# Optimization experiments

Measured on AMD Instinct MI355X. Metric: run time of the kernel, lower is better.

## Reference

```python
import jax, jax.numpy as jnp
import numpy as np

B, S, H = 4, 2048, 1024
NH, HD = 16, 64
ROPE_THETA = 160000.0
SCALE = HD ** -0.5


def _rope_cos_sin(position_ids, dim, theta):
    # neox-style rotary: frequencies over half the head dim
    inv_freq = 1.0 / (theta ** (jnp.arange(0, dim, 2, dtype=jnp.float32) / dim))  # [dim/2]
    freqs = position_ids.astype(jnp.float32)[..., None] * inv_freq  # [B,S,dim/2]
    return jnp.cos(freqs), jnp.sin(freqs)


def _apply_rope(x, cos, sin):
    # x: [B,S,NH,HD]; neox style: rotate halves
    d2 = x.shape[-1] // 2
    x1, x2 = x[..., :d2], x[..., d2:]
    c = cos[:, :, None, :]
    s = sin[:, :, None, :]
    return jnp.concatenate([x1 * c - x2 * s, x2 * c + x1 * s], axis=-1)


def setup_inputs() -> dict:
    key = jax.random.key(0)
    k1, k2, k3 = jax.random.split(key, 3)
    hidden_states = jax.random.normal(k1, (B, S, H), dtype=jnp.float32)
    position_ids = jnp.tile(jnp.arange(S, dtype=jnp.int32)[None, :], (B, 1))
    Wqkv = jax.random.normal(k2, (3 * H, H), dtype=jnp.float32) * (H ** -0.5)
    Wo = jax.random.normal(k3, (H, H), dtype=jnp.float32) * (H ** -0.5)
    return {"hidden_states": hidden_states, "position_ids": position_ids,
            "Wqkv": Wqkv, "Wo": Wo}


def reference(hidden_states, position_ids, Wqkv, Wo):
    # fused QKV projection
    qkv = jnp.einsum('bsh,oh->bso', hidden_states, Wqkv)  # [B,S,3H]
    q, k, v = jnp.split(qkv, 3, axis=-1)
    q = q.reshape(B, S, NH, HD)
    k = k.reshape(B, S, NH, HD)
    v = v.reshape(B, S, NH, HD)
    # rotary embedding (neox style)
    cos, sin = _rope_cos_sin(position_ids, HD, ROPE_THETA)
    q = _apply_rope(q, cos, sin)
    k = _apply_rope(k, cos, sin)
    # full bidirectional (encoder-only, global layer) attention
    scores = jnp.einsum('bqhd,bkhd->bhqk', q, k) * SCALE  # [B,NH,S,S]
    probs = jax.nn.softmax(scores, axis=-1)
    ctx = jnp.einsum('bhqk,bkhd->bqhd', probs, v).reshape(B, S, H)
    # output projection
    return jnp.einsum('bsh,oh->bso', ctx, Wo)
```

## Files before the change

### kernel.cpp

```cpp
#include <hip/hip_runtime.h>
#include <hip/hip_bf16.h>


#define GLOBAL_AS __attribute__((address_space(1)))
#define LDS_AS    __attribute__((address_space(3)))

using f32x4  = __attribute__((ext_vector_type(4))) float;
using f32x16 = __attribute__((ext_vector_type(16))) float;
using s16x8  = __attribute__((ext_vector_type(8))) short;

__device__ __forceinline__ void gld_lds16(const void* g, void* l) {
  __builtin_amdgcn_global_load_lds((const GLOBAL_AS void*)g, (LDS_AS void*)l, 16, 0, 0);
}

__device__ __forceinline__ unsigned short f2bf(float f) {
  unsigned int u = __float_as_uint(f);
  u = (u + 0x7fffu + ((u >> 16) & 1u)) >> 16;
  return (unsigned short)u;
}
__device__ __forceinline__ unsigned int cvt_pk_bf16(float lo, float hi) {
  unsigned int r;
  asm("v_cvt_pk_bf16_f32 %0, %1, %2" : "=v"(r) : "v"(lo), "v"(hi));
  return r;
}
__device__ __forceinline__ void pswap(unsigned int& a, unsigned int& b) {
  asm("v_permlane32_swap_b32 %0, %1" : "+v"(a), "+v"(b));
}

__global__ __launch_bounds__(256) void cvt_rope_kernel(const float* __restrict__ h,
                                                       const float* __restrict__ wq,
                                                       const float* __restrict__ wo,
                                                       const int* __restrict__ pos,
                                                       unsigned short* __restrict__ hb,
                                                       unsigned short* __restrict__ wqb,
                                                       unsigned short* __restrict__ wob,
                                                       float* __restrict__ ctab,
                                                       float* __restrict__ stab) {
  int b = blockIdx.x;
  if (b >= 12288) {
    int idx = (b - 12288) * 256 + threadIdx.x;
    int d = idx & 31;
    int bs = idx >> 5;
    float p = (float)pos[bs];
    float inv = exp2f(-(float)d * 0.5402410118609203f);
    float f = p * inv;
    ctab[idx] = cosf(f);
    stab[idx] = sinf(f);
    return;
  }
  const float* src; unsigned short* dst; int i;
  if (b < 8192)       { src = h;  dst = hb;  i = b * 256 + threadIdx.x; }
  else if (b < 11264) { src = wq; dst = wqb; i = (b - 8192) * 256 + threadIdx.x; }
  else                { src = wo; dst = wob; i = (b - 11264) * 256 + threadIdx.x; }
  float4 v = ((const float4*)src)[i];
  ushort4 o;
  o.x = f2bf(v.x); o.y = f2bf(v.y); o.z = f2bf(v.z); o.w = f2bf(v.w);
  ((ushort4*)dst)[i] = o;
}

template<int MODE>
__global__ __launch_bounds__(512) void gemm2_kernel(const unsigned short* __restrict__ A,
                                                    const unsigned short* __restrict__ Bm,
                                                    void* __restrict__ C, int N, int K,
                                                    const float* __restrict__ ctab,
                                                    const float* __restrict__ stab,
                                                    unsigned short* __restrict__ Qr,
                                                    unsigned short* __restrict__ Kr,
                                                    unsigned short* __restrict__ Vt) {
  extern __shared__ char lds[];
  const int tid  = threadIdx.x;
  const int lane = tid & 63, w = tid >> 6;
  const int g = lane >> 4, c = lane & 15;
  const int wr = w >> 1, wc = w & 1;
  const int m0 = blockIdx.x * 256, n0 = blockIdx.y * 128;
  const char* Ab = (const char*)A;
  const char* Bb = (const char*)Bm;
  const int NKT = K >> 6;

#define STAGE_A(kt, hh)                                                          \
  {                                                                              \
    _Pragma("unroll")                                                            \
    for (int L = 0; L < 2; ++L) {                                                \
      int o = tid * 16 + L * 8192;                                               \
      int row = o >> 7;                                                          \
      int gcol = (o & 127) ^ ((row & 7) << 4);                                   \
      gld_lds16(Ab + ((size_t)(m0 + (hh) * 128 + row) * K + (kt) * 64) * 2 + gcol,\
                lds + ((kt) & 1) * 49152 + (hh) * 16384 + o);                    \
    }                                                                            \
  }
#define STAGE_B(kt, hh)                                                          \
  {                                                                              \
    int o = tid * 16;                                                            \
    int row = o >> 7;                                                            \
    int gcol = (o & 127) ^ ((row & 7) << 4);                                     \
    gld_lds16(Bb + ((size_t)(n0 + (hh) * 64 + row) * K + (kt) * 64) * 2 + gcol,  \
              lds + ((kt) & 1) * 49152 + 32768 + (hh) * 8192 + o);               \
  }

  STAGE_A(0, 0); STAGE_B(0, 0); STAGE_A(0, 1); STAGE_B(0, 1);
  __builtin_amdgcn_sched_barrier(0);
  STAGE_A(1, 0); STAGE_B(1, 0);
  __builtin_amdgcn_sched_barrier(0);

  f32x4 acc[4][4] = {};
  const int rA0 = (wr & 1) * 64 + c;
  for (int kt = 0; kt < NKT; ++kt) {
    if (kt == NKT - 1) asm volatile("s_waitcnt vmcnt(0)" ::: "memory");
    else               asm volatile("s_waitcnt vmcnt(3)" ::: "memory");
    __builtin_amdgcn_sched_barrier(0);
    __builtin_amdgcn_s_barrier();
    __builtin_amdgcn_sched_barrier(0);

    const char* baseA = lds + (kt & 1) * 49152 + (wr >> 1) * 16384;
    const char* baseB = lds + (kt & 1) * 49152 + 32768 + wc * 8192;

    s16x8 af[4][2], bf[4][2];
#pragma unroll
    for (int i = 0; i < 4; ++i) {
      int row = rA0 + 16 * i;
#pragma unroll
      for (int ks = 0; ks < 2; ++ks)
        af[i][ks] = *(const s16x8*)(baseA + ((row * 128 + ks * 64 + g * 16) ^ ((row & 7) << 4)));
    }
#pragma unroll
    for (int j = 0; j < 4; ++j) {
      int row = 16 * j + c;
#pragma unroll
      for (int ks = 0; ks < 2; ++ks)
        bf[j][ks] = *(const s16x8*)(baseB + ((row * 128 + ks * 64 + g * 16) ^ ((row & 7) << 4)));
    }

    if (kt + 1 < NKT) {
      STAGE_A(kt + 1, 1);
      STAGE_B(kt + 1, 1);
    }
    __builtin_amdgcn_sched_barrier(0);

    __builtin_amdgcn_s_setprio(1);
#pragma unroll
    for (int ks = 0; ks < 2; ++ks)
#pragma unroll
      for (int i = 0; i < 4; ++i)
#pragma unroll
        for (int j = 0; j < 4; ++j)
          acc[i][j] = __builtin_amdgcn_mfma_f32_16x16x32_bf16(af[i][ks], bf[j][ks], acc[i][j], 0, 0, 0);
    __builtin_amdgcn_s_setprio(0);

    __builtin_amdgcn_sched_barrier(0);
    __builtin_amdgcn_s_barrier();
    __builtin_amdgcn_sched_barrier(0);
    if (kt + 2 < NKT) {
      STAGE_A(kt + 2, 0);
      STAGE_B(kt + 2, 0);
      __builtin_amdgcn_sched_barrier(0);
    }
  }
#undef STAGE_A
#undef STAGE_B

  if (MODE == 1) {
#pragma unroll
    for (int i = 0; i < 4; ++i)
#pragma unroll
      for (int j = 0; j < 4; ++j)
#pragma unroll
        for (int r = 0; r < 4; ++r) {
          int m = m0 + wr * 64 + 16 * i + 4 * g + r;
          int n = n0 + wc * 64 + 16 * j + c;
          ((float*)C)[(size_t)m * N + n] = acc[i][j][r];
        }
  } else {
    const int t = blockIdx.y;
    if (t < 16) {
      unsigned short* dstb = (t < 8) ? Qr : Kr;
      const float qs = (t < 8) ? 0.18033688011112042f : 1.0f;
      const int h = 2 * (t & 7) + wc;
#pragma unroll
      for (int i = 0; i < 4; ++i)
#pragma unroll
        for (int r = 0; r < 4; ++r) {
          int m = m0 + wr * 64 + 16 * i + 4 * g + r;
          int b = m >> 11, s = m & 2047;
          unsigned short* drow = dstb + ((size_t)(b * 16 + h) * 2048 + s) * 64;
#pragma unroll
          for (int j = 0; j < 2; ++j) {
            int d = 16 * j + c;
            float co = ctab[(size_t)m * 32 + d];
            float si = stab[(size_t)m * 32 + d];
            float x1 = acc[i][j][r], x2 = acc[i][j + 2][r];
            drow[d]      = f2bf((x1 * co - x2 * si) * qs);
            drow[d + 32] = f2bf((x2 * co + x1 * si) * qs);
          }
        }
    } else {
      unsigned short (*tile)[72] = (unsigned short (*)[72])lds;
      const int bb = m0 >> 11, sb = m0 & 2047;
#pragma unroll
      for (int hp = 0; hp < 2; ++hp) {
        __syncthreads();
        if (wc == hp) {
#pragma unroll
          for (int i = 0; i < 4; ++i)
#pragma unroll
            for (int j = 0; j < 4; ++j)
#pragma unroll
              for (int r = 0; r < 4; ++r)
                tile[wr * 64 + 16 * i + 4 * g + r][16 * j + c] = f2bf(acc[i][j][r]);
        }
        __syncthreads();
        int hh = 2 * (t - 16) + hp;
        int d = tid >> 3, p = tid & 7;
        alignas(16) unsigned short vv[32];
#pragma unroll
        for (int i2 = 0; i2 < 32; ++i2) vv[i2] = tile[p * 32 + i2][d];
        unsigned short* dst = Vt + ((size_t)(bb * 16 + hh) * 64 + d) * 2048 + sb + p * 32;
#pragma unroll
        for (int q4 = 0; q4 < 4; ++q4)
          *(uint4*)(dst + 8 * q4) = ((const uint4*)vv)[q4];
      }
    }
  }
}

__global__ __launch_bounds__(512) void attn_kernel(const unsigned short* __restrict__ Q,
                                                   const unsigned short* __restrict__ Kr,
                                                   const unsigned short* __restrict__ Vt,
                                                   unsigned short* __restrict__ Ctx) {
  __shared__ char sK[3][8192];
  __shared__ char sV[3][8192];
  const int tid  = threadIdx.x;
  const int lane = tid & 63, w = tid >> 6;
  const int hi = lane >> 5, ql = lane & 31;
  const int swz = (ql & 7) << 4;
  int lin = blockIdx.x + 8 * blockIdx.y;
  int eff = (lin & 7) * 64 + (lin >> 3);
  const int bh = eff >> 3;
  const int q0 = (eff & 7) * 256;
  const char* kh = (const char*)(Kr + (size_t)bh * 2048 * 64);
  const char* vh = (const char*)(Vt + (size_t)bh * 64 * 2048);

  s16x8 qf[4];
  {
    const char* qrow = (const char*)Q + ((size_t)bh * 2048 + q0 + 32 * w + ql) * 128;
#pragma unroll
    for (int t = 0; t < 4; ++t) qf[t] = *(const s16x8*)(qrow + t * 32 + hi * 16);
  }
  __builtin_amdgcn_sched_barrier(0);

#define STAGE(t, b)                                                              \
  {                                                                              \
    int o = tid * 16;                                                            \
    int l = o ^ (((o >> 7) & 7) << 4);                                           \
    gld_lds16(kh + (size_t)(t) * 8192 + l, sK[b] + o);                           \
    gld_lds16(vh + (size_t)(o >> 7) * 4096 + (t) * 128 + (l & 127), sV[b] + o);  \
  }

  STAGE(0, 0);
  __builtin_amdgcn_sched_barrier(0);
  STAGE(1, 1);
  __builtin_amdgcn_sched_barrier(0);

  float l_run = 0.f;
  f32x16 oa0 = {}, oa1 = {};
  int cur = 0;

  for (int it = 0; it < 32; ++it) {
    if (it == 0 || it == 31) asm volatile("s_waitcnt vmcnt(0)" ::: "memory");
    else                     asm volatile("s_waitcnt vmcnt(2)" ::: "memory");
    __builtin_amdgcn_sched_barrier(0);
    __builtin_amdgcn_s_barrier();
    __builtin_amdgcn_sched_barrier(0);

    if (it + 2 < 32) {
      int sb = cur + 2; if (sb >= 3) sb -= 3;
      STAGE(it + 2, sb);
    }
    __builtin_amdgcn_sched_barrier(0);

    f32x16 sc0 = {}, sc1 = {};
    __builtin_amdgcn_s_setprio(1);
#pragma unroll
    for (int t = 0; t < 4; ++t) {
      int cx = (t * 32 + hi * 16) ^ swz;
      s16x8 k0 = *(const s16x8*)(sK[cur] + ql * 128 + cx);
      s16x8 k1 = *(const s16x8*)(sK[cur] + (32 + ql) * 128 + cx);
      sc0 = __builtin_amdgcn_mfma_f32_32x32x16_bf16(k0, qf[t], sc0, 0, 0, 0);
      sc1 = __builtin_amdgcn_mfma_f32_32x32x16_bf16(k1, qf[t], sc1, 0, 0, 0);
    }
    __builtin_amdgcn_s_setprio(0);

    float rs = 0.f;
#pragma unroll
    for (int r = 0; r < 16; ++r) { sc0[r] = __builtin_amdgcn_exp2f(sc0[r]); rs += sc0[r]; }
#pragma unroll
    for (int r = 0; r < 16; ++r) { sc1[r] = __builtin_amdgcn_exp2f(sc1[r]); rs += sc1[r]; }
    l_run += rs;

    unsigned int bp[16];
#pragma unroll
    for (int blk = 0; blk < 2; ++blk) {
      const f32x16& s = blk ? sc1 : sc0;
      unsigned int a0 = cvt_pk_bf16(s[0],  s[1]);
      unsigned int a1 = cvt_pk_bf16(s[2],  s[3]);
      unsigned int a2 = cvt_pk_bf16(s[4],  s[5]);
      unsigned int a3 = cvt_pk_bf16(s[6],  s[7]);
      pswap(a0, a2); pswap(a1, a3);
      bp[blk * 8 + 0] = a0; bp[blk * 8 + 1] = a1;
      bp[blk * 8 + 2] = a2; bp[blk * 8 + 3] = a3;
      unsigned int b0 = cvt_pk_bf16(s[8],  s[9]);
      unsigned int b1 = cvt_pk_bf16(s[10], s[11]);
      unsigned int b2 = cvt_pk_bf16(s[12], s[13]);
      unsigned int b3 = cvt_pk_bf16(s[14], s[15]);
      pswap(b0, b2); pswap(b1, b3);
      bp[blk * 8 + 4] = b0; bp[blk * 8 + 5] = b1;
      bp[blk * 8 + 6] = b2; bp[blk * 8 + 7] = b3;
    }

    __builtin_amdgcn_s_setprio(1);
#pragma unroll
    for (int ss = 0; ss < 4; ++ss) {
      uint4 u = {bp[ss * 4], bp[ss * 4 + 1], bp[ss * 4 + 2], bp[ss * 4 + 3]};
      s16x8 pb = __builtin_bit_cast(s16x8, u);
      int cx = (ss * 32 + hi * 16) ^ swz;
      s16x8 v0 = *(const s16x8*)(sV[cur] + ql * 128 + cx);
      s16x8 v1 = *(const s16x8*)(sV[cur] + (32 + ql) * 128 + cx);
      oa0 = __builtin_amdgcn_mfma_f32_32x32x16_bf16(v0, pb, oa0, 0, 0, 0);
      oa1 = __builtin_amdgcn_mfma_f32_32x32x16_bf16(v1, pb, oa1, 0, 0, 0);
    }
    __builtin_amdgcn_s_setprio(0);

    ++cur; if (cur == 3) cur = 0;
  }
#undef STAGE

  l_run += __shfl_xor(l_run, 32);
  float inv = 1.f / l_run;
  const int b = bh >> 4, h = bh & 15;
  const int q = q0 + 32 * w + ql;
  unsigned short* crow = Ctx + ((size_t)(b * 2048 + q)) * 1024 + h * 64;
#pragma unroll
  for (int dblk = 0; dblk < 2; ++dblk) {
    const f32x16& oa = dblk ? oa1 : oa0;
#pragma unroll
    for (int grp = 0; grp < 4; ++grp) {
      ushort4 st;
      st.x = f2bf(oa[4 * grp + 0] * inv);
      st.y = f2bf(oa[4 * grp + 1] * inv);
      st.z = f2bf(oa[4 * grp + 2] * inv);
      st.w = f2bf(oa[4 * grp + 3] * inv);
      *(ushort4*)(crow + dblk * 32 + 8 * grp + 4 * hi) = st;
    }
  }
}

extern "C" void kernel_launch(void* const* d_in, const int* in_sizes, int n_in,
                              void* d_out, int out_size, void* d_ws, size_t ws_size,
                              hipStream_t stream) {
  const float* hidden = (const float*)d_in[0];
  const int*   pos    = (const int*)d_in[1];
  const float* wqkv   = (const float*)d_in[2];
  const float* wo     = (const float*)d_in[3];

  char* ws = (char*)d_ws;
  unsigned short* hbf  = (unsigned short*)(ws);
  unsigned short* wqbf = (unsigned short*)(ws + 16777216);
  unsigned short* wobf = (unsigned short*)(ws + 23068672);
  unsigned short* Qr   = (unsigned short*)(ws + 41943040);
  unsigned short* Kr   = (unsigned short*)(ws + 58720256);
  unsigned short* Vt   = (unsigned short*)(ws + 75497472);
  unsigned short* ctx  = (unsigned short*)(ws + 92274688);
  float*          ctab = (float*)(ws + 109051904);
  float*          stab = (float*)(ws + 110100480);

  cvt_rope_kernel<<<13312, 256, 0, stream>>>(hidden, wqkv, wo, pos,
                                             hbf, wqbf, wobf, ctab, stab);

  dim3 gq(32, 24);
  gemm2_kernel<2><<<gq, 512, 98304, stream>>>(hbf, wqbf, nullptr, 3072, 1024,
                                              ctab, stab, Qr, Kr, Vt);

  dim3 ga(8, 64);
  attn_kernel<<<ga, 512, 0, stream>>>(Qr, Kr, Vt, ctx);

  dim3 go(32, 8);
  gemm2_kernel<1><<<go, 512, 98304, stream>>>(ctx, wobf, d_out, 1024, 1024,
                                              nullptr, nullptr, nullptr, nullptr, nullptr);
}
```

Measured before the change: 184.9 us.

## Shrink GEMM tile to 256x64 with one head per block for more blocks

The QKV and output-projection GEMMs drop from 256x128 tiles to 256x64. Each of the 8 waves now owns a 32x64 slice, the B tile is a single 64-row stage, and LDS per block falls to 80 KB. The grid doubles, so there are more blocks to spread across CUs, and each block maps to exactly one head, which simplifies the RoPE and V-transpose epilogue to a single pass. The cost is less reuse of A per block, so more global and L2 traffic per FLOP, and fewer MFMAs per LDS read.

```diff
diff --git a/kernel.cpp b/kernel.cpp
--- a/kernel.cpp
+++ b/kernel.cpp
@@ -59,65 +59,63 @@
 }
 
 template<int MODE>
-__global__ __launch_bounds__(512) void gemm2_kernel(const unsigned short* __restrict__ A,
-                                                    const unsigned short* __restrict__ Bm,
-                                                    void* __restrict__ C, int N, int K,
-                                                    const float* __restrict__ ctab,
-                                                    const float* __restrict__ stab,
-                                                    unsigned short* __restrict__ Qr,
-                                                    unsigned short* __restrict__ Kr,
-                                                    unsigned short* __restrict__ Vt) {
+__global__ __launch_bounds__(512, 4) void gemm2_kernel(const unsigned short* __restrict__ A,
+                                                       const unsigned short* __restrict__ Bm,
+                                                       void* __restrict__ C, int N, int K,
+                                                       const float* __restrict__ ctab,
+                                                       const float* __restrict__ stab,
+                                                       unsigned short* __restrict__ Qr,
+                                                       unsigned short* __restrict__ Kr,
+                                                       unsigned short* __restrict__ Vt) {
   extern __shared__ char lds[];
   const int tid  = threadIdx.x;
   const int lane = tid & 63, w = tid >> 6;
   const int g = lane >> 4, c = lane & 15;
-  const int wr = w >> 1, wc = w & 1;
-  const int m0 = blockIdx.x * 256, n0 = blockIdx.y * 128;
+  const int m0 = blockIdx.x * 256, n0 = blockIdx.y * 64;
   const char* Ab = (const char*)A;
   const char* Bb = (const char*)Bm;
   const int NKT = K >> 6;
 
-#define STAGE_A(kt, hh)                                                          \
-  {                                                                              \
-    _Pragma("unroll")                                                            \
-    for (int L = 0; L < 2; ++L) {                                                \
-      int o = tid * 16 + L * 8192;                                               \
-      int row = o >> 7;                                                          \
-      int gcol = (o & 127) ^ ((row & 7) << 4);                                   \
+#define STAGE_A(kt, hh)                                                           \
+  {                                                                               \
+    _Pragma("unroll")                                                             \
+    for (int L = 0; L < 2; ++L) {                                                 \
+      int o = tid * 16 + L * 8192;                                                \
+      int row = o >> 7;                                                           \
+      int gcol = (o & 127) ^ ((row & 7) << 4);                                    \
       gld_lds16(Ab + ((size_t)(m0 + (hh) * 128 + row) * K + (kt) * 64) * 2 + gcol,\
-                lds + ((kt) & 1) * 49152 + (hh) * 16384 + o);                    \
-    }                                                                            \
-  }
-#define STAGE_B(kt, hh)                                                          \
-  {                                                                              \
-    int o = tid * 16;                                                            \
-    int row = o >> 7;                                                            \
-    int gcol = (o & 127) ^ ((row & 7) << 4);                                     \
-    gld_lds16(Bb + ((size_t)(n0 + (hh) * 64 + row) * K + (kt) * 64) * 2 + gcol,  \
-              lds + ((kt) & 1) * 49152 + 32768 + (hh) * 8192 + o);               \
-  }
-
-  STAGE_A(0, 0); STAGE_B(0, 0); STAGE_A(0, 1); STAGE_B(0, 1);
-  __builtin_amdgcn_sched_barrier(0);
-  STAGE_A(1, 0); STAGE_B(1, 0);
-  __builtin_amdgcn_sched_barrier(0);
-
-  f32x4 acc[4][4] = {};
-  const int rA0 = (wr & 1) * 64 + c;
+                lds + ((kt) & 1) * 40960 + (hh) * 16384 + o);                     \
+    }                                                                             \
+  }
+#define STAGE_B(kt)                                                               \
+  {                                                                               \
+    int o = tid * 16;                                                             \
+    int row = o >> 7;                                                             \
+    int gcol = (o & 127) ^ ((row & 7) << 4);                                      \
+    gld_lds16(Bb + ((size_t)(n0 + row) * K + (kt) * 64) * 2 + gcol,               \
+              lds + ((kt) & 1) * 40960 + 32768 + o);                              \
+  }
+
+  STAGE_A(0, 0); STAGE_A(0, 1); STAGE_B(0);
+  __builtin_amdgcn_sched_barrier(0);
+  STAGE_A(1, 0);
+  __builtin_amdgcn_sched_barrier(0);
+
+  f32x4 acc[2][4] = {};
   for (int kt = 0; kt < NKT; ++kt) {
     if (kt == NKT - 1) asm volatile("s_waitcnt vmcnt(0)" ::: "memory");
-    else               asm volatile("s_waitcnt vmcnt(3)" ::: "memory");
+    else               asm volatile("s_waitcnt vmcnt(2)" ::: "memory");
     __builtin_amdgcn_sched_barrier(0);
     __builtin_amdgcn_s_barrier();
     __builtin_amdgcn_sched_barrier(0);
 
-    const char* baseA = lds + (kt & 1) * 49152 + (wr >> 1) * 16384;
-    const char* baseB = lds + (kt & 1) * 49152 + 32768 + wc * 8192;
-
-    s16x8 af[4][2], bf[4][2];
-#pragma unroll
-    for (int i = 0; i < 4; ++i) {
-      int row = rA0 + 16 * i;
+    const char* baseA = lds + (kt & 1) * 40960;
+    const char* baseB = baseA + 32768;
+
+    s16x8 af[2][2], bf[4][2];
+#pragma unroll
+    for (int i = 0; i < 2; ++i) {
+      int row = w * 32 + 16 * i + c;
 #pragma unroll
       for (int ks = 0; ks < 2; ++ks)
         af[i][ks] = *(const s16x8*)(baseA + ((row * 128 + ks * 64 + g * 16) ^ ((row & 7) << 4)));
@@ -132,7 +130,7 @@
 
     if (kt + 1 < NKT) {
       STAGE_A(kt + 1, 1);
-      STAGE_B(kt + 1, 1);
+      STAGE_B(kt + 1);
     }
     __builtin_amdgcn_sched_barrier(0);
 
@@ -140,7 +138,7 @@
 #pragma unroll
     for (int ks = 0; ks < 2; ++ks)
 #pragma unroll
-      for (int i = 0; i < 4; ++i)
+      for (int i = 0; i < 2; ++i)
 #pragma unroll
         for (int j = 0; j < 4; ++j)
           acc[i][j] = __builtin_amdgcn_mfma_f32_16x16x32_bf16(af[i][ks], bf[j][ks], acc[i][j], 0, 0, 0);
@@ -151,7 +149,6 @@
     __builtin_amdgcn_sched_barrier(0);
     if (kt + 2 < NKT) {
       STAGE_A(kt + 2, 0);
-      STAGE_B(kt + 2, 0);
       __builtin_amdgcn_sched_barrier(0);
     }
   }
@@ -160,26 +157,26 @@
 
   if (MODE == 1) {
 #pragma unroll
-    for (int i = 0; i < 4; ++i)
+    for (int i = 0; i < 2; ++i)
 #pragma unroll
       for (int j = 0; j < 4; ++j)
 #pragma unroll
         for (int r = 0; r < 4; ++r) {
-          int m = m0 + wr * 64 + 16 * i + 4 * g + r;
-          int n = n0 + wc * 64 + 16 * j + c;
+          int m = m0 + w * 32 + 16 * i + 4 * g + r;
+          int n = n0 + 16 * j + c;
           ((float*)C)[(size_t)m * N + n] = acc[i][j][r];
         }
   } else {
     const int t = blockIdx.y;
-    if (t < 16) {
-      unsigned short* dstb = (t < 8) ? Qr : Kr;
-      const float qs = (t < 8) ? 0.18033688011112042f : 1.0f;
-      const int h = 2 * (t & 7) + wc;
-#pragma unroll
-      for (int i = 0; i < 4; ++i)
+    if (t < 32) {
+      unsigned short* dstb = (t < 16) ? Qr : Kr;
+      const float qs = (t < 16) ? 0.18033688011112042f : 1.0f;
+      const int h = t & 15;
+#pragma unroll
+      for (int i = 0; i < 2; ++i)
 #pragma unroll
         for (int r = 0; r < 4; ++r) {
-          int m = m0 + wr * 64 + 16 * i + 4 * g + r;
+          int m = m0 + w * 32 + 16 * i + 4 * g + r;
           int b = m >> 11, s = m & 2047;
           unsigned short* drow = dstb + ((size_t)(b * 16 + h) * 2048 + s) * 64;
 #pragma unroll
@@ -195,29 +192,23 @@
     } else {
       unsigned short (*tile)[72] = (unsigned short (*)[72])lds;
       const int bb = m0 >> 11, sb = m0 & 2047;
-#pragma unroll
-      for (int hp = 0; hp < 2; ++hp) {
-        __syncthreads();
-        if (wc == hp) {
-#pragma unroll
-          for (int i = 0; i < 4; ++i)
-#pragma unroll
-            for (int j = 0; j < 4; ++j)
-#pragma unroll
-              for (int r = 0; r < 4; ++r)
-                tile[wr * 64 + 16 * i + 4 * g + r][16 * j + c] = f2bf(acc[i][j][r]);
-        }
-        __syncthreads();
-        int hh = 2 * (t - 16) + hp;
-        int d = tid >> 3, p = tid & 7;
-        alignas(16) unsigned short vv[32];
-#pragma unroll
-        for (int i2 = 0; i2 < 32; ++i2) vv[i2] = tile[p * 32 + i2][d];
-        unsigned short* dst = Vt + ((size_t)(bb * 16 + hh) * 64 + d) * 2048 + sb + p * 32;
-#pragma unroll
-        for (int q4 = 0; q4 < 4; ++q4)
-          *(uint4*)(dst + 8 * q4) = ((const uint4*)vv)[q4];
-      }
+      const int h = t - 32;
+#pragma unroll
+      for (int i = 0; i < 2; ++i)
+#pragma unroll
+        for (int j = 0; j < 4; ++j)
+#pragma unroll
+          for (int r = 0; r < 4; ++r)
+            tile[w * 32 + 16 * i + 4 * g + r][16 * j + c] = f2bf(acc[i][j][r]);
+      __syncthreads();
+      int d = tid >> 3, p = tid & 7;
+      alignas(16) unsigned short vv[32];
+#pragma unroll
+      for (int i2 = 0; i2 < 32; ++i2) vv[i2] = tile[p * 32 + i2][d];
+      unsigned short* dst = Vt + ((size_t)(bb * 16 + h) * 64 + d) * 2048 + sb + p * 32;
+#pragma unroll
+      for (int q4 = 0; q4 < 4; ++q4)
+        *(uint4*)(dst + 8 * q4) = ((const uint4*)vv)[q4];
     }
   }
 }
@@ -375,14 +366,14 @@
   cvt_rope_kernel<<<13312, 256, 0, stream>>>(hidden, wqkv, wo, pos,
                                              hbf, wqbf, wobf, ctab, stab);
 
-  dim3 gq(32, 24);
-  gemm2_kernel<2><<<gq, 512, 98304, stream>>>(hbf, wqbf, nullptr, 3072, 1024,
+  dim3 gq(32, 48);
+  gemm2_kernel<2><<<gq, 512, 81920, stream>>>(hbf, wqbf, nullptr, 3072, 1024,
                                               ctab, stab, Qr, Kr, Vt);
 
   dim3 ga(8, 64);
   attn_kernel<<<ga, 512, 0, stream>>>(Qr, Kr, Vt, ctx);
 
-  dim3 go(32, 8);
-  gemm2_kernel<1><<<go, 512, 98304, stream>>>(ctx, wobf, d_out, 1024, 1024,
+  dim3 go(32, 16);
+  gemm2_kernel<1><<<go, 512, 81920, stream>>>(ctx, wobf, d_out, 1024, 1024,
                                               nullptr, nullptr, nullptr, nullptr, nullptr);
 }
```

Result: no change. 183.1 us (-1.0%).

## Split QKV GEMM K-loop into interleaved phases and add smaller-tile output GEMM

Applied to the files above, without the earlier changes.

The QKV projection kernel now splits each K-tile into four MFMA phases, with LDS fragment loads and next-tile global-to-LDS staging interleaved between them and extra barriers between phases. The goal is to overlap memory traffic with matrix-core work and to reduce the number of fragments live in registers at once. The output projection now runs on a separate 256-thread kernel with 256x64 tiles, which launches twice as many blocks and allows two blocks per CU to improve occupancy on that small GEMM. In exchange there are more s_barrier calls per iteration and the per-phase wait and staging ordering gets more complex.

```diff
diff --git a/kernel.cpp b/kernel.cpp
--- a/kernel.cpp
+++ b/kernel.cpp
@@ -58,10 +58,9 @@
   ((ushort4*)dst)[i] = o;
 }
 
-template<int MODE>
-__global__ __launch_bounds__(512) void gemm2_kernel(const unsigned short* __restrict__ A,
+__global__ __launch_bounds__(512) void gemm8_kernel(const unsigned short* __restrict__ A,
                                                     const unsigned short* __restrict__ Bm,
-                                                    void* __restrict__ C, int N, int K,
+                                                    int N, int K,
                                                     const float* __restrict__ ctab,
                                                     const float* __restrict__ stab,
                                                     unsigned short* __restrict__ Qr,
@@ -114,36 +113,80 @@
     const char* baseA = lds + (kt & 1) * 49152 + (wr >> 1) * 16384;
     const char* baseB = lds + (kt & 1) * 49152 + 32768 + wc * 8192;
 
-    s16x8 af[4][2], bf[4][2];
-#pragma unroll
-    for (int i = 0; i < 4; ++i) {
-      int row = rA0 + 16 * i;
-#pragma unroll
-      for (int ks = 0; ks < 2; ++ks)
-        af[i][ks] = *(const s16x8*)(baseA + ((row * 128 + ks * 64 + g * 16) ^ ((row & 7) << 4)));
-    }
+    s16x8 b0[4], aP[2];
 #pragma unroll
     for (int j = 0; j < 4; ++j) {
       int row = 16 * j + c;
-#pragma unroll
-      for (int ks = 0; ks < 2; ++ks)
-        bf[j][ks] = *(const s16x8*)(baseB + ((row * 128 + ks * 64 + g * 16) ^ ((row & 7) << 4)));
-    }
-
-    if (kt + 1 < NKT) {
-      STAGE_A(kt + 1, 1);
-      STAGE_B(kt + 1, 1);
-    }
-    __builtin_amdgcn_sched_barrier(0);
-
-    __builtin_amdgcn_s_setprio(1);
-#pragma unroll
-    for (int ks = 0; ks < 2; ++ks)
-#pragma unroll
-      for (int i = 0; i < 4; ++i)
-#pragma unroll
-        for (int j = 0; j < 4; ++j)
-          acc[i][j] = __builtin_amdgcn_mfma_f32_16x16x32_bf16(af[i][ks], bf[j][ks], acc[i][j], 0, 0, 0);
+      b0[j] = *(const s16x8*)(baseB + ((row * 128 + g * 16) ^ ((row & 7) << 4)));
+    }
+#pragma unroll
+    for (int i = 0; i < 2; ++i) {
+      int row = rA0 + 16 * i;
+      aP[i] = *(const s16x8*)(baseA + ((row * 128 + g * 16) ^ ((row & 7) << 4)));
+    }
+    if (kt + 1 < NKT) STAGE_A(kt + 1, 1);
+    __builtin_amdgcn_sched_barrier(0);
+    __builtin_amdgcn_s_barrier();
+    __builtin_amdgcn_s_setprio(1);
+#pragma unroll
+    for (int i = 0; i < 2; ++i)
+#pragma unroll
+      for (int j = 0; j < 4; ++j)
+        acc[i][j] = __builtin_amdgcn_mfma_f32_16x16x32_bf16(aP[i], b0[j], acc[i][j], 0, 0, 0);
+    __builtin_amdgcn_s_setprio(0);
+
+    s16x8 aQ[2];
+#pragma unroll
+    for (int i = 0; i < 2; ++i) {
+      int row = rA0 + 16 * (i + 2);
+      aQ[i] = *(const s16x8*)(baseA + ((row * 128 + g * 16) ^ ((row & 7) << 4)));
+    }
+    if (kt + 1 < NKT) STAGE_B(kt + 1, 1);
+    __builtin_amdgcn_sched_barrier(0);
+    __builtin_amdgcn_s_barrier();
+    __builtin_amdgcn_s_setprio(1);
+#pragma unroll
+    for (int i = 0; i < 2; ++i)
+#pragma unroll
+      for (int j = 0; j < 4; ++j)
+        acc[i + 2][j] = __builtin_amdgcn_mfma_f32_16x16x32_bf16(aQ[i], b0[j], acc[i + 2][j], 0, 0, 0);
+    __builtin_amdgcn_s_setprio(0);
+
+    s16x8 b1[4], aR[2];
+#pragma unroll
+    for (int j = 0; j < 4; ++j) {
+      int row = 16 * j + c;
+      b1[j] = *(const s16x8*)(baseB + ((row * 128 + 64 + g * 16) ^ ((row & 7) << 4)));
+    }
+#pragma unroll
+    for (int i = 0; i < 2; ++i) {
+      int row = rA0 + 16 * i;
+      aR[i] = *(const s16x8*)(baseA + ((row * 128 + 64 + g * 16) ^ ((row & 7) << 4)));
+    }
+    __builtin_amdgcn_sched_barrier(0);
+    __builtin_amdgcn_s_barrier();
+    __builtin_amdgcn_s_setprio(1);
+#pragma unroll
+    for (int i = 0; i < 2; ++i)
+#pragma unroll
+      for (int j = 0; j < 4; ++j)
+        acc[i][j] = __builtin_amdgcn_mfma_f32_16x16x32_bf16(aR[i], b1[j], acc[i][j], 0, 0, 0);
+    __builtin_amdgcn_s_setprio(0);
+
+    s16x8 aS[2];
+#pragma unroll
+    for (int i = 0; i < 2; ++i) {
+      int row = rA0 + 16 * (i + 2);
+      aS[i] = *(const s16x8*)(baseA + ((row * 128 + 64 + g * 16) ^ ((row & 7) << 4)));
+    }
+    __builtin_amdgcn_sched_barrier(0);
+    __builtin_amdgcn_s_barrier();
+    __builtin_amdgcn_s_setprio(1);
+#pragma unroll
+    for (int i = 0; i < 2; ++i)
+#pragma unroll
+      for (int j = 0; j < 4; ++j)
+        acc[i + 2][j] = __builtin_amdgcn_mfma_f32_16x16x32_bf16(aS[i], b1[j], acc[i + 2][j], 0, 0, 0);
     __builtin_amdgcn_s_setprio(0);
 
     __builtin_amdgcn_sched_barrier(0);
@@ -158,68 +201,161 @@
 #undef STAGE_A
 #undef STAGE_B
 
-  if (MODE == 1) {
+  const int t = blockIdx.y;
+  if (t < 16) {
+    unsigned short* dstb = (t < 8) ? Qr : Kr;
+    const float qs = (t < 8) ? 0.18033688011112042f : 1.0f;
+    const int h = 2 * (t & 7) + wc;
 #pragma unroll
     for (int i = 0; i < 4; ++i)
 #pragma unroll
-      for (int j = 0; j < 4; ++j)
-#pragma unroll
-        for (int r = 0; r < 4; ++r) {
-          int m = m0 + wr * 64 + 16 * i + 4 * g + r;
-          int n = n0 + wc * 64 + 16 * j + c;
-          ((float*)C)[(size_t)m * N + n] = acc[i][j][r];
+      for (int r = 0; r < 4; ++r) {
+        int m = m0 + wr * 64 + 16 * i + 4 * g + r;
+        int b = m >> 11, s = m & 2047;
+        unsigned short* drow = dstb + ((size_t)(b * 16 + h) * 2048 + s) * 64;
+#pragma unroll
+        for (int j = 0; j < 2; ++j) {
+          int d = 16 * j + c;
+          float co = ctab[(size_t)m * 32 + d];
+          float si = stab[(size_t)m * 32 + d];
+          float x1 = acc[i][j][r], x2 = acc[i][j + 2][r];
+          drow[d]      = f2bf((x1 * co - x2 * si) * qs);
+          drow[d + 32] = f2bf((x2 * co + x1 * si) * qs);
         }
+      }
   } else {
-    const int t = blockIdx.y;
-    if (t < 16) {
-      unsigned short* dstb = (t < 8) ? Qr : Kr;
-      const float qs = (t < 8) ? 0.18033688011112042f : 1.0f;
-      const int h = 2 * (t & 7) + wc;
+    unsigned short (*tile)[72] = (unsigned short (*)[72])lds;
+    const int bb = m0 >> 11, sb = m0 & 2047;
+#pragma unroll
+    for (int hp = 0; hp < 2; ++hp) {
+      __syncthreads();
+      if (wc == hp) {
+#pragma unroll
+        for (int i = 0; i < 4; ++i)
+#pragma unroll
+          for (int j = 0; j < 4; ++j)
+#pragma unroll
+            for (int r = 0; r < 4; ++r)
+              tile[wr * 64 + 16 * i + 4 * g + r][16 * j + c] = f2bf(acc[i][j][r]);
+      }
+      __syncthreads();
+      int hh = 2 * (t - 16) + hp;
+      int d = tid >> 3, p = tid & 7;
+      alignas(16) unsigned short vv[32];
+#pragma unroll
+      for (int i2 = 0; i2 < 32; ++i2) vv[i2] = tile[p * 32 + i2][d];
+      unsigned short* dst = Vt + ((size_t)(bb * 16 + hh) * 64 + d) * 2048 + sb + p * 32;
+#pragma unroll
+      for (int q4 = 0; q4 < 4; ++q4)
+        *(uint4*)(dst + 8 * q4) = ((const uint4*)vv)[q4];
+    }
+  }
+}
+
+__global__ __launch_bounds__(256, 2) void gemm3_kernel(const unsigned short* __restrict__ A,
+                                                       const unsigned short* __restrict__ Bm,
+                                                       float* __restrict__ C, int N, int K) {
+  extern __shared__ char lds[];
+  const int tid  = threadIdx.x;
+  const int lane = tid & 63, w = tid >> 6;
+  const int g = lane >> 4, c = lane & 15;
+  const int m0 = blockIdx.x * 256, n0 = blockIdx.y * 64;
+  const char* Ab = (const char*)A;
+  const char* Bb = (const char*)Bm;
+  const int NKT = K >> 6;
+
+#define STAGE_A(kt, hh)                                                           \
+  {                                                                               \
+    _Pragma("unroll")                                                             \
+    for (int L = 0; L < 4; ++L) {                                                 \
+      int o = tid * 16 + L * 4096;                                                \
+      int row = o >> 7;                                                           \
+      int gcol = (o & 127) ^ ((row & 7) << 4);                                    \
+      gld_lds16(Ab + ((size_t)(m0 + (hh) * 128 + row) * K + (kt) * 64) * 2 + gcol,\
+                lds + ((kt) & 1) * 40960 + (hh) * 16384 + o);                     \
+    }                                                                             \
+  }
+#define STAGE_B(kt)                                                               \
+  {                                                                               \
+    _Pragma("unroll")                                                             \
+    for (int L = 0; L < 2; ++L) {                                                 \
+      int o = tid * 16 + L * 4096;                                                \
+      int row = o >> 7;                                                           \
+      int gcol = (o & 127) ^ ((row & 7) << 4);                                    \
+      gld_lds16(Bb + ((size_t)(n0 + row) * K + (kt) * 64) * 2 + gcol,             \
+                lds + ((kt) & 1) * 40960 + 32768 + o);                            \
+    }                                                                             \
+  }
+
+  STAGE_A(0, 0); STAGE_A(0, 1); STAGE_B(0);
+  __builtin_amdgcn_sched_barrier(0);
+  STAGE_A(1, 0);
+  __builtin_amdgcn_sched_barrier(0);
+
+  f32x4 acc[4][4] = {};
+  for (int kt = 0; kt < NKT; ++kt) {
+    if (kt == 0 || kt == NKT - 1) asm volatile("s_waitcnt vmcnt(0)" ::: "memory");
+    else                          asm volatile("s_waitcnt vmcnt(4)" ::: "memory");
+    __builtin_amdgcn_sched_barrier(0);
+    __builtin_amdgcn_s_barrier();
+    __builtin_amdgcn_sched_barrier(0);
+
+    const char* baseA = lds + (kt & 1) * 40960;
+    const char* baseB = baseA + 32768;
+
+    s16x8 af[4][2], bf[4][2];
+#pragma unroll
+    for (int i = 0; i < 4; ++i) {
+      int row = w * 64 + 16 * i + c;
+#pragma unroll
+      for (int ks = 0; ks < 2; ++ks)
+        af[i][ks] = *(const s16x8*)(baseA + ((row * 128 + ks * 64 + g * 16) ^ ((row & 7) << 4)));
+    }
+#pragma unroll
+    for (int j = 0; j < 4; ++j) {
+      int row = 16 * j + c;
+#pragma unroll
+      for (int ks = 0; ks < 2; ++ks)
+        bf[j][ks] = *(const s16x8*)(baseB + ((row * 128 + ks * 64 + g * 16) ^ ((row & 7) << 4)));
+    }
+
+    if (kt + 1 < NKT) {
+      STAGE_A(kt + 1, 1);
+      STAGE_B(kt + 1);
+    }
+    __builtin_amdgcn_sched_barrier(0);
+
+    __builtin_amdgcn_s_setprio(1);
+#pragma unroll
+    for (int ks = 0; ks < 2; ++ks)
 #pragma unroll
       for (int i = 0; i < 4; ++i)
 #pragma unroll
-        for (int r = 0; r < 4; ++r) {
-          int m = m0 + wr * 64 + 16 * i + 4 * g + r;
-          int b = m >> 11, s = m & 2047;
-          unsigned short* drow = dstb + ((size_t)(b * 16 + h) * 2048 + s) * 64;
-#pragma unroll
-          for (int j = 0; j < 2; ++j) {
-            int d = 16 * j + c;
-            float co = ctab[(size_t)m * 32 + d];
-            float si = stab[(size_t)m * 32 + d];
-            float x1 = acc[i][j][r], x2 = acc[i][j + 2][r];
-            drow[d]      = f2bf((x1 * co - x2 * si) * qs);
-            drow[d + 32] = f2bf((x2 * co + x1 * si) * qs);
-          }
-        }
-    } else {
-      unsigned short (*tile)[72] = (unsigned short (*)[72])lds;
-      const int bb = m0 >> 11, sb = m0 & 2047;
-#pragma unroll
-      for (int hp = 0; hp < 2; ++hp) {
-        __syncthreads();
-        if (wc == hp) {
-#pragma unroll
-          for (int i = 0; i < 4; ++i)
-#pragma unroll
-            for (int j = 0; j < 4; ++j)
-#pragma unroll
-              for (int r = 0; r < 4; ++r)
-                tile[wr * 64 + 16 * i + 4 * g + r][16 * j + c] = f2bf(acc[i][j][r]);
-        }
-        __syncthreads();
-        int hh = 2 * (t - 16) + hp;
-        int d = tid >> 3, p = tid & 7;
-        alignas(16) unsigned short vv[32];
-#pragma unroll
-        for (int i2 = 0; i2 < 32; ++i2) vv[i2] = tile[p * 32 + i2][d];
-        unsigned short* dst = Vt + ((size_t)(bb * 16 + hh) * 64 + d) * 2048 + sb + p * 32;
-#pragma unroll
-        for (int q4 = 0; q4 < 4; ++q4)
-          *(uint4*)(dst + 8 * q4) = ((const uint4*)vv)[q4];
+        for (int j = 0; j < 4; ++j)
+          acc[i][j] = __builtin_amdgcn_mfma_f32_16x16x32_bf16(af[i][ks], bf[j][ks], acc[i][j], 0, 0, 0);
+    __builtin_amdgcn_s_setprio(0);
+
+    __builtin_amdgcn_sched_barrier(0);
+    __builtin_amdgcn_s_barrier();
+    __builtin_amdgcn_sched_barrier(0);
+    if (kt + 2 < NKT) {
+      STAGE_A(kt + 2, 0);
+      __builtin_amdgcn_sched_barrier(0);
+    }
+  }
+#undef STAGE_A
+#undef STAGE_B
+
+#pragma unroll
+  for (int i = 0; i < 4; ++i)
+#pragma unroll
+    for (int j = 0; j < 4; ++j)
+#pragma unroll
+      for (int r = 0; r < 4; ++r) {
+        int m = m0 + w * 64 + 16 * i + 4 * g + r;
+        int n = n0 + 16 * j + c;
+        C[(size_t)m * N + n] = acc[i][j][r];
       }
-    }
-  }
 }
 
 __global__ __launch_bounds__(512) void attn_kernel(const unsigned short* __restrict__ Q,
@@ -376,13 +512,12 @@
                                              hbf, wqbf, wobf, ctab, stab);
 
   dim3 gq(32, 24);
-  gemm2_kernel<2><<<gq, 512, 98304, stream>>>(hbf, wqbf, nullptr, 3072, 1024,
-                                              ctab, stab, Qr, Kr, Vt);
+  gemm8_kernel<<<gq, 512, 98304, stream>>>(hbf, wqbf, 3072, 1024,
+                                           ctab, stab, Qr, Kr, Vt);
 
   dim3 ga(8, 64);
   attn_kernel<<<ga, 512, 0, stream>>>(Qr, Kr, Vt, ctx);
 
-  dim3 go(32, 8);
-  gemm2_kernel<1><<<go, 512, 98304, stream>>>(ctx, wobf, d_out, 1024, 1024,
-                                              nullptr, nullptr, nullptr, nullptr, nullptr);
-}
+  dim3 go(32, 16);
+  gemm3_kernel<<<go, 256, 81920, stream>>>(ctx, wobf, (float*)d_out, 1024, 1024);
+}
```

Result: no change. 187.4 us (+1.3%).
